# Performance work log

Hardware: AMD Instinct MI355X
Metric: run time of the kernel (lower is better)

Reference implementation:

```python
import jax, jax.numpy as jnp
import numpy as np

B, T, D = 4, 2048, 1024
H = 16
HD = D // H

def setup_inputs() -> dict:
    key = jax.random.key(0)
    ks = jax.random.split(key, 3)
    x = jax.random.normal(ks[0], (B, T, D), dtype=jnp.float32)
    w_qkv = jax.random.normal(ks[1], (D, 3 * D), dtype=jnp.float32) * (1.0 / np.sqrt(D))
    b_qkv = jnp.zeros((3 * D,), dtype=jnp.float32)
    w_proj = jax.random.normal(ks[2], (D, D), dtype=jnp.float32) * (1.0 / np.sqrt(D))
    b_proj = jnp.zeros((D,), dtype=jnp.float32)
    return {"x": x, "w_qkv": w_qkv, "b_qkv": b_qkv, "w_proj": w_proj, "b_proj": b_proj}

def reference(x, w_qkv, b_qkv, w_proj, b_proj):
    b, t, c = x.shape
    qkv = x @ w_qkv + b_qkv                      # [B,T,3D]
    qkv = qkv.reshape(b, t, 3, H, HD).transpose(2, 0, 3, 1, 4)  # [3,B,H,T,HD]
    q, k, v = qkv[0], qkv[1], qkv[2]
    scale = jnp.sqrt(jnp.asarray(HD, dtype=x.dtype))
    attn = jnp.einsum('bhqd,bhkd->bhqk', q, k) / scale  # [B,H,T,T]
    causal = jnp.tril(jnp.ones((t, t), dtype=bool))
    attn = jnp.where(causal[None, None], attn, -jnp.inf)
    attn = jax.nn.softmax(attn, axis=-1)
    out = jnp.einsum('bhqk,bhkd->bhqd', attn, v)        # [B,H,T,HD]
    out = out.transpose(0, 2, 1, 3).reshape(b, t, c)
    return out @ w_proj + b_proj
```

## Files before the change

kernel.cpp:

```cpp
#include <hip/hip_runtime.h>

typedef float f32x4 __attribute__((ext_vector_type(4)));
typedef __bf16 bf16x8 __attribute__((ext_vector_type(8)));

static __device__ __forceinline__ unsigned short f2bf(float f) {
    unsigned int u = __builtin_bit_cast(unsigned int, f);
    u += 0x7fffu + ((u >> 16) & 1u);
    return (unsigned short)(u >> 16);
}
static __device__ __forceinline__ unsigned short bfc(float f) {
    return __builtin_bit_cast(unsigned short, (__bf16)f);
}

#define QSC 0.18033688011112042f

typedef const __attribute__((address_space(1))) unsigned int gu32;
typedef __attribute__((address_space(3))) unsigned int lu32;
static __device__ __forceinline__ void gload_lds16(const unsigned short* g, unsigned short* l) {
    __builtin_amdgcn_global_load_lds((gu32*)g, (lu32*)l, 16, 0, 0);
}

__global__ __launch_bounds__(256)
void cvt_bf16(const float* __restrict__ in, unsigned short* __restrict__ out) {
    int i = blockIdx.x * 256 + threadIdx.x;
    const float4* p = (const float4*)in + (size_t)i * 2;
    float4 a = p[0], b = p[1];
    union { unsigned short s[8]; uint4 v; } u;
    u.s[0] = f2bf(a.x); u.s[1] = f2bf(a.y); u.s[2] = f2bf(a.z); u.s[3] = f2bf(a.w);
    u.s[4] = f2bf(b.x); u.s[5] = f2bf(b.y); u.s[6] = f2bf(b.z); u.s[7] = f2bf(b.w);
    ((uint4*)out)[i] = u.v;
}

__global__ __launch_bounds__(256)
void transpose_w(const float* __restrict__ w, unsigned short* __restrict__ wT,
                 int K, int N) {
    __shared__ unsigned short Lt[64][65];
    const int k0 = blockIdx.x * 64, n0 = blockIdx.y * 64;
    const int t = threadIdx.x;
    const int r = t >> 4, c4 = (t & 15) * 4;
    #pragma unroll
    for (int i = 0; i < 4; i++) {
        int rr = r + i * 16;
        float4 v = *(const float4*)(w + (k0 + rr) * N + n0 + c4);
        Lt[rr][c4 + 0] = f2bf(v.x); Lt[rr][c4 + 1] = f2bf(v.y);
        Lt[rr][c4 + 2] = f2bf(v.z); Lt[rr][c4 + 3] = f2bf(v.w);
    }
    __syncthreads();
    const int rn = t >> 3, ks = (t & 7) * 8;
    #pragma unroll
    for (int i = 0; i < 2; i++) {
        int rr = rn + i * 32;
        unsigned short tmp[8];
        #pragma unroll
        for (int j = 0; j < 8; j++) tmp[j] = Lt[ks + j][rr];
        *(uint4*)(wT + (n0 + rr) * K + k0 + ks) = *(const uint4*)tmp;
    }
}

__global__ __launch_bounds__(256)
void qkv_gemm2(const unsigned short* __restrict__ A,
               const unsigned short* __restrict__ Bt,
               const float* __restrict__ bias,
               unsigned short* __restrict__ q_ws,
               unsigned short* __restrict__ k_ws,
               unsigned short* __restrict__ vT_ws)
{
    const int K = 1024;
    __shared__ unsigned short Al[128 * 32];
    __shared__ unsigned short Bl[128 * 32];
    const int tid = threadIdx.x;
    const int lane = tid & 63, w = tid >> 6;
    const int l15 = lane & 15, lhi = lane >> 4;
    const int m0 = blockIdx.x * 128, n0 = blockIdx.y * 128;
    const int wm = (w >> 1) * 64, wn = (w & 1) * 64;

    const int srow = w * 32 + (lane >> 2);
    const int sslot = lane & 3;
    const unsigned short* ga = A + (size_t)(m0 + srow) * K + sslot * 8;
    const unsigned short* gb = Bt + (size_t)(n0 + srow) * K + sslot * 8;
    unsigned short* la = Al + w * 32 * 32;
    unsigned short* lb = Bl + w * 32 * 32;

    f32x4 acc[4][4] = {};

    for (int k0 = 0; k0 < K; k0 += 32) {
        __syncthreads();
        gload_lds16(ga + k0,          la);
        gload_lds16(ga + k0 + 16 * K, la + 16 * 32);
        gload_lds16(gb + k0,          lb);
        gload_lds16(gb + k0 + 16 * K, lb + 16 * 32);
        __syncthreads();
        bf16x8 af[4], bfr[4];
        #pragma unroll
        for (int m = 0; m < 4; m++)
            af[m] = *(const bf16x8*)(Al + (wm + m * 16 + l15) * 32 + lhi * 8);
        #pragma unroll
        for (int n = 0; n < 4; n++)
            bfr[n] = *(const bf16x8*)(Bl + (wn + n * 16 + l15) * 32 + lhi * 8);
        #pragma unroll
        for (int m = 0; m < 4; m++)
            #pragma unroll
            for (int n = 0; n < 4; n++)
                acc[m][n] = __builtin_amdgcn_mfma_f32_16x16x32_bf16(af[m], bfr[n], acc[m][n], 0, 0, 0);
    }

    #pragma unroll
    for (int n = 0; n < 4; n++) {
        int col = n0 + wn + n * 16 + l15;
        float bv = bias[col];
        int which = col >> 10;
        int d = col & 1023;
        int h = d >> 6, hd = d & 63;
        #pragma unroll
        for (int m = 0; m < 4; m++) {
            #pragma unroll
            for (int j = 0; j < 4; j++) {
                int row = m0 + wm + m * 16 + lhi * 4 + j;
                int b = row >> 11, t = row & 2047;
                float val = acc[m][n][j] + bv;
                int bh = b * 16 + h;
                if (which == 0)      q_ws[(bh * 2048 + t) * 64 + hd] = f2bf(val * QSC);
                else if (which == 1) k_ws[(bh * 2048 + t) * 64 + hd] = f2bf(val);
                else                 vT_ws[(bh * 64 + hd) * 2048 + t] = f2bf(val);
            }
        }
    }
}

#define LKK 72

__global__ __launch_bounds__(512, 4)
void attn_fwd(const unsigned short* __restrict__ q_ws,
              const unsigned short* __restrict__ k_ws,
              const unsigned short* __restrict__ vT_ws,
              unsigned short* __restrict__ attn_ws)
{
    __shared__ unsigned short Kb[2][64 * LKK];
    __shared__ unsigned short Vb[2][64 * LKK];
    __shared__ unsigned short Pl[8][16 * 64];

    const int bh = blockIdx.x;
    const int p  = blockIdx.y;
    const int b = bh >> 4, h = bh & 15;
    const int tid = threadIdx.x;
    const int lane = tid & 63, wid = tid >> 6;
    const int l15 = lane & 15, lhi = lane >> 4;
    const int tbase = bh * 2048;
    const float NINF = -__builtin_inff();

    const int r0 = tid >> 3;
    const int c0 = (tid & 7) * 8;
    const unsigned short* kg = k_ws + (size_t)(tbase + r0) * 64 + c0;
    const unsigned short* vg = vT_ws + ((size_t)bh * 64 + r0) * 2048 + c0;

    unsigned short* Pw = &Pl[wid][0];
    const int xr = l15 & 7;

    #pragma unroll 1
    for (int seg = 0; seg < 2; ++seg) {
        const int qb = seg ? p : 15 - p;
        const int q0 = qb * 128;
        const int qrow = q0 + wid * 16;
        const int nkv = 2 * (qb + 1);

        bf16x8 qf[2];
        #pragma unroll
        for (int ks = 0; ks < 2; ks++)
            qf[ks] = *(const bf16x8*)(q_ws + (size_t)(tbase + qrow + l15) * 64 + ks * 32 + lhi * 8);

        f32x4 o[4] = {};
        float mreg = NINF, lst = 0.f;

        {
            uint4 ka = *(const uint4*)(kg);
            uint4 va = *(const uint4*)(vg);
            *(uint4*)(&Kb[0][r0 * LKK + c0]) = ka;
            *(uint4*)(&Vb[0][r0 * LKK + c0]) = va;
        }
        __syncthreads();

        int cur = 0;
        for (int kb = 0; kb < nkv; ++kb) {
            const int k0 = kb * 64;
            const int knx = (kb + 1 < nkv ? kb + 1 : kb) * 64;
            uint4 ka = *(const uint4*)(kg + (size_t)knx * 64);
            uint4 va = *(const uint4*)(vg + knx);

            if (k0 <= qrow + 15) {
                f32x4 s[4] = {};
                __builtin_amdgcn_s_setprio(1);
                #pragma unroll
                for (int ks = 0; ks < 2; ks++) {
                    bf16x8 kf[4];
                    #pragma unroll
                    for (int n = 0; n < 4; n++)
                        kf[n] = *(const bf16x8*)(&Kb[cur][(n * 16 + l15) * LKK + ks * 32 + lhi * 8]);
                    #pragma unroll
                    for (int n = 0; n < 4; n++)
                        s[n] = __builtin_amdgcn_mfma_f32_16x16x32_bf16(kf[n], qf[ks], s[n], 0, 0, 0);
                }
                __builtin_amdgcn_s_setprio(0);
                if (k0 + 63 > qrow) {
                    int qg = qrow + l15;
                    #pragma unroll
                    for (int n = 0; n < 4; n++) {
                        int kgl = k0 + n * 16 + lhi * 4;
                        #pragma unroll
                        for (int j = 0; j < 4; j++)
                            s[n][j] = (kgl + j <= qg) ? s[n][j] : NINF;
                    }
                }
                float mx = NINF;
                #pragma unroll
                for (int n = 0; n < 4; n++)
                    #pragma unroll
                    for (int j = 0; j < 4; j++)
                        mx = fmaxf(mx, s[n][j]);
                mx = fmaxf(mx, __shfl_xor(mx, 16));
                mx = fmaxf(mx, __shfl_xor(mx, 32));

                if (__all(mx <= mreg + 8.f)) {
                    float rs = 0.f;
                    #pragma unroll
                    for (int n = 0; n < 4; n++)
                        #pragma unroll
                        for (int j = 0; j < 4; j++) {
                            float pv = exp2f(s[n][j] - mreg);
                            s[n][j] = pv;
                            rs += pv;
                        }
                    rs += __shfl_xor(rs, 16);
                    rs += __shfl_xor(rs, 32);
                    lst += rs;
                } else {
                    float mnew = fmaxf(mreg, mx);
                    float al = exp2f(mreg - mnew);
                    mreg = mnew;
                    float rs = 0.f;
                    #pragma unroll
                    for (int n = 0; n < 4; n++)
                        #pragma unroll
                        for (int j = 0; j < 4; j++) {
                            float pv = exp2f(s[n][j] - mnew);
                            s[n][j] = pv;
                            rs += pv;
                        }
                    rs += __shfl_xor(rs, 16);
                    rs += __shfl_xor(rs, 32);
                    lst = lst * al + rs;
                    #pragma unroll
                    for (int j = 0; j < 4; j++) {
                        float a = __shfl(al, lhi * 4 + j);
                        #pragma unroll
                        for (int nd = 0; nd < 4; nd++)
                            o[nd][j] *= a;
                    }
                }
                #pragma unroll
                for (int n = 0; n < 4; n++) {
                    ushort4 pk;
                    pk.x = bfc(s[n][0]); pk.y = bfc(s[n][1]);
                    pk.z = bfc(s[n][2]); pk.w = bfc(s[n][3]);
                    int chunk = (2 * n + (lhi >> 1)) ^ xr;
                    *(ushort4*)(&Pw[l15 * 64 + chunk * 8 + (lhi & 1) * 4]) = pk;
                }
                __builtin_amdgcn_s_setprio(1);
                #pragma unroll
                for (int ks = 0; ks < 2; ks++) {
                    int chunk = (4 * ks + lhi) ^ xr;
                    bf16x8 pf = *(const bf16x8*)(&Pw[l15 * 64 + chunk * 8]);
                    bf16x8 vf[4];
                    #pragma unroll
                    for (int nd = 0; nd < 4; nd++)
                        vf[nd] = *(const bf16x8*)(&Vb[cur][(nd * 16 + l15) * LKK + ks * 32 + lhi * 8]);
                    #pragma unroll
                    for (int nd = 0; nd < 4; nd++)
                        o[nd] = __builtin_amdgcn_mfma_f32_16x16x32_bf16(pf, vf[nd], o[nd], 0, 0, 0);
                }
                __builtin_amdgcn_s_setprio(0);
            }
            *(uint4*)(&Kb[cur ^ 1][r0 * LKK + c0]) = ka;
            *(uint4*)(&Vb[cur ^ 1][r0 * LKK + c0]) = va;
            __syncthreads();
            cur ^= 1;
        }
        #pragma unroll
        for (int j = 0; j < 4; j++) {
            float lv = __shfl(lst, lhi * 4 + j);
            float inv = 1.0f / lv;
            int t = qrow + lhi * 4 + j;
            #pragma unroll
            for (int nd = 0; nd < 4; nd++) {
                int d = nd * 16 + l15;
                attn_ws[((size_t)(b * 2048 + t) * 16 + h) * 64 + d] = f2bf(o[nd][j] * inv);
            }
        }
    }
}

__global__ __launch_bounds__(256)
void proj_gemm2(const unsigned short* __restrict__ A,
                const unsigned short* __restrict__ Bt,
                const float* __restrict__ bias, float* __restrict__ out)
{
    const int K = 1024, N = 1024;
    __shared__ unsigned short Al[128 * 32];
    __shared__ unsigned short Bl[128 * 32];
    const int tid = threadIdx.x;
    const int lane = tid & 63, w = tid >> 6;
    const int l15 = lane & 15, lhi = lane >> 4;
    const int m0 = blockIdx.x * 128, n0 = blockIdx.y * 128;
    const int wm = (w >> 1) * 64, wn = (w & 1) * 64;

    const int srow = w * 32 + (lane >> 2);
    const int sslot = lane & 3;
    const unsigned short* ga = A + (size_t)(m0 + srow) * K + sslot * 8;
    const unsigned short* gb = Bt + (size_t)(n0 + srow) * K + sslot * 8;
    unsigned short* la = Al + w * 32 * 32;
    unsigned short* lb = Bl + w * 32 * 32;

    f32x4 acc[4][4] = {};

    for (int k0 = 0; k0 < K; k0 += 32) {
        __syncthreads();
        gload_lds16(ga + k0,          la);
        gload_lds16(ga + k0 + 16 * K, la + 16 * 32);
        gload_lds16(gb + k0,          lb);
        gload_lds16(gb + k0 + 16 * K, lb + 16 * 32);
        __syncthreads();
        bf16x8 af[4], bfr[4];
        #pragma unroll
        for (int m = 0; m < 4; m++)
            af[m] = *(const bf16x8*)(Al + (wm + m * 16 + l15) * 32 + lhi * 8);
        #pragma unroll
        for (int n = 0; n < 4; n++)
            bfr[n] = *(const bf16x8*)(Bl + (wn + n * 16 + l15) * 32 + lhi * 8);
        #pragma unroll
        for (int m = 0; m < 4; m++)
            #pragma unroll
            for (int n = 0; n < 4; n++)
                acc[m][n] = __builtin_amdgcn_mfma_f32_16x16x32_bf16(af[m], bfr[n], acc[m][n], 0, 0, 0);
    }

    #pragma unroll
    for (int n = 0; n < 4; n++) {
        int col = n0 + wn + n * 16 + l15;
        float bv = bias[col];
        #pragma unroll
        for (int m = 0; m < 4; m++)
            #pragma unroll
            for (int j = 0; j < 4; j++) {
                int row = m0 + wm + m * 16 + lhi * 4 + j;
                out[row * N + col] = acc[m][n][j] + bv;
            }
    }
}

extern "C" void kernel_launch(void* const* d_in, const int* in_sizes, int n_in,
                              void* d_out, int out_size, void* d_ws, size_t ws_size,
                              hipStream_t stream)
{
    const float* x      = (const float*)d_in[0];
    const float* w_qkv  = (const float*)d_in[1];
    const float* b_qkv  = (const float*)d_in[2];
    const float* w_proj = (const float*)d_in[3];
    const float* b_proj = (const float*)d_in[4];
    float* out = (float*)d_out;

    const size_t SEG = (size_t)8 * 1024 * 1024;
    unsigned short* q_ws    = (unsigned short*)d_ws;
    unsigned short* k_ws    = q_ws + SEG;
    unsigned short* vT_ws   = k_ws + SEG;
    unsigned short* attn_ws = vT_ws + SEG;

    unsigned short* x_bf   = (unsigned short*)d_out;
    unsigned short* wqkvT  = x_bf + SEG;
    unsigned short* wprojT = q_ws;

    cvt_bf16<<<4096, 256, 0, stream>>>(x, x_bf);
    transpose_w<<<dim3(16, 48), 256, 0, stream>>>(w_qkv, wqkvT, 1024, 3072);
    qkv_gemm2<<<dim3(64, 24), 256, 0, stream>>>(x_bf, wqkvT, b_qkv, q_ws, k_ws, vT_ws);
    attn_fwd<<<dim3(64, 8), 512, 0, stream>>>(q_ws, k_ws, vT_ws, attn_ws);
    transpose_w<<<dim3(16, 16), 256, 0, stream>>>(w_proj, wprojT, 1024, 1024);
    proj_gemm2<<<dim3(64, 8), 256, 0, stream>>>(attn_ws, wprojT, b_proj, out);
}
```

Baseline: 201.4 us.

## Double-buffer LDS tiles in QKV and projection GEMMs with MFMA priority boost

Both bf16 GEMM kernels now keep two LDS buffers per operand and prefetch the next k-tile with global_load_lds while MFMAs run on the current one. This replaces two barriers per iteration with one and is meant to hide global-load latency behind compute. It also raises wave priority around the MFMA block with s_setprio. LDS use doubles to 32 KB per block, which may lower occupancy. Correctness depends on the compiler inserting a vmcnt wait before the barrier so the async LDS writes are complete.

New measurement: 199.5 us. No clear change (-0.9%).

```diff
diff --git a/kernel.cpp b/kernel.cpp
--- a/kernel.cpp
+++ b/kernel.cpp
@@ -66,8 +66,8 @@
                unsigned short* __restrict__ vT_ws)
 {
     const int K = 1024;
-    __shared__ unsigned short Al[128 * 32];
-    __shared__ unsigned short Bl[128 * 32];
+    __shared__ unsigned short Al[2][128 * 32];
+    __shared__ unsigned short Bl[2][128 * 32];
     const int tid = threadIdx.x;
     const int lane = tid & 63, w = tid >> 6;
     const int l15 = lane & 15, lhi = lane >> 4;
@@ -78,30 +78,41 @@
     const int sslot = lane & 3;
     const unsigned short* ga = A + (size_t)(m0 + srow) * K + sslot * 8;
     const unsigned short* gb = Bt + (size_t)(n0 + srow) * K + sslot * 8;
-    unsigned short* la = Al + w * 32 * 32;
-    unsigned short* lb = Bl + w * 32 * 32;
+    const int lofs = w * 32 * 32;
 
     f32x4 acc[4][4] = {};
 
+    gload_lds16(ga, &Al[0][lofs]);
+    gload_lds16(ga + 16 * K, &Al[0][lofs + 512]);
+    gload_lds16(gb, &Bl[0][lofs]);
+    gload_lds16(gb + 16 * K, &Bl[0][lofs + 512]);
+    __syncthreads();
+
+    int cur = 0;
     for (int k0 = 0; k0 < K; k0 += 32) {
-        __syncthreads();
-        gload_lds16(ga + k0,          la);
-        gload_lds16(ga + k0 + 16 * K, la + 16 * 32);
-        gload_lds16(gb + k0,          lb);
-        gload_lds16(gb + k0 + 16 * K, lb + 16 * 32);
-        __syncthreads();
+        const int nxt = cur ^ 1;
+        if (k0 + 32 < K) {
+            gload_lds16(ga + k0 + 32,          &Al[nxt][lofs]);
+            gload_lds16(ga + k0 + 32 + 16 * K, &Al[nxt][lofs + 512]);
+            gload_lds16(gb + k0 + 32,          &Bl[nxt][lofs]);
+            gload_lds16(gb + k0 + 32 + 16 * K, &Bl[nxt][lofs + 512]);
+        }
         bf16x8 af[4], bfr[4];
         #pragma unroll
         for (int m = 0; m < 4; m++)
-            af[m] = *(const bf16x8*)(Al + (wm + m * 16 + l15) * 32 + lhi * 8);
+            af[m] = *(const bf16x8*)(&Al[cur][(wm + m * 16 + l15) * 32 + lhi * 8]);
         #pragma unroll
         for (int n = 0; n < 4; n++)
-            bfr[n] = *(const bf16x8*)(Bl + (wn + n * 16 + l15) * 32 + lhi * 8);
+            bfr[n] = *(const bf16x8*)(&Bl[cur][(wn + n * 16 + l15) * 32 + lhi * 8]);
+        __builtin_amdgcn_s_setprio(1);
         #pragma unroll
         for (int m = 0; m < 4; m++)
             #pragma unroll
             for (int n = 0; n < 4; n++)
                 acc[m][n] = __builtin_amdgcn_mfma_f32_16x16x32_bf16(af[m], bfr[n], acc[m][n], 0, 0, 0);
+        __builtin_amdgcn_s_setprio(0);
+        __syncthreads();
+        cur = nxt;
     }
 
     #pragma unroll
@@ -304,8 +315,8 @@
                 const float* __restrict__ bias, float* __restrict__ out)
 {
     const int K = 1024, N = 1024;
-    __shared__ unsigned short Al[128 * 32];
-    __shared__ unsigned short Bl[128 * 32];
+    __shared__ unsigned short Al[2][128 * 32];
+    __shared__ unsigned short Bl[2][128 * 32];
     const int tid = threadIdx.x;
     const int lane = tid & 63, w = tid >> 6;
     const int l15 = lane & 15, lhi = lane >> 4;
@@ -316,30 +327,41 @@
     const int sslot = lane & 3;
     const unsigned short* ga = A + (size_t)(m0 + srow) * K + sslot * 8;
     const unsigned short* gb = Bt + (size_t)(n0 + srow) * K + sslot * 8;
-    unsigned short* la = Al + w * 32 * 32;
-    unsigned short* lb = Bl + w * 32 * 32;
+    const int lofs = w * 32 * 32;
 
     f32x4 acc[4][4] = {};
 
+    gload_lds16(ga, &Al[0][lofs]);
+    gload_lds16(ga + 16 * K, &Al[0][lofs + 512]);
+    gload_lds16(gb, &Bl[0][lofs]);
+    gload_lds16(gb + 16 * K, &Bl[0][lofs + 512]);
+    __syncthreads();
+
+    int cur = 0;
     for (int k0 = 0; k0 < K; k0 += 32) {
-        __syncthreads();
-        gload_lds16(ga + k0,          la);
-        gload_lds16(ga + k0 + 16 * K, la + 16 * 32);
-        gload_lds16(gb + k0,          lb);
-        gload_lds16(gb + k0 + 16 * K, lb + 16 * 32);
-        __syncthreads();
+        const int nxt = cur ^ 1;
+        if (k0 + 32 < K) {
+            gload_lds16(ga + k0 + 32,          &Al[nxt][lofs]);
+            gload_lds16(ga + k0 + 32 + 16 * K, &Al[nxt][lofs + 512]);
+            gload_lds16(gb + k0 + 32,          &Bl[nxt][lofs]);
+            gload_lds16(gb + k0 + 32 + 16 * K, &Bl[nxt][lofs + 512]);
+        }
         bf16x8 af[4], bfr[4];
         #pragma unroll
         for (int m = 0; m < 4; m++)
-            af[m] = *(const bf16x8*)(Al + (wm + m * 16 + l15) * 32 + lhi * 8);
+            af[m] = *(const bf16x8*)(&Al[cur][(wm + m * 16 + l15) * 32 + lhi * 8]);
         #pragma unroll
         for (int n = 0; n < 4; n++)
-            bfr[n] = *(const bf16x8*)(Bl + (wn + n * 16 + l15) * 32 + lhi * 8);
+            bfr[n] = *(const bf16x8*)(&Bl[cur][(wn + n * 16 + l15) * 32 + lhi * 8]);
+        __builtin_amdgcn_s_setprio(1);
         #pragma unroll
         for (int m = 0; m < 4; m++)
             #pragma unroll
             for (int n = 0; n < 4; n++)
                 acc[m][n] = __builtin_amdgcn_mfma_f32_16x16x32_bf16(af[m], bfr[n], acc[m][n], 0, 0, 0);
+        __builtin_amdgcn_s_setprio(0);
+        __syncthreads();
+        cur = nxt;
     }
 
     #pragma unroll
```
